# Performance work log

Hardware: AMD Instinct MI355X
Metric: run time of the kernel (lower is better)

The kernel has to match this reference:

```python
import jax, jax.numpy as jnp
import numpy as np

INPUT_DIMS = 512
OUTPUT_DIMS = 512
GRID_SIZE = 8


def setup_inputs() -> dict:
    key = jax.random.key(0)
    k_x, k_w = jax.random.split(key)
    x = jax.random.normal(k_x, (4, 2048, INPUT_DIMS), dtype=jnp.float32)
    scale = 1.0 / (np.sqrt(INPUT_DIMS) * np.sqrt(GRID_SIZE))
    fouriercoeffs = jax.random.normal(
        k_w, (2, OUTPUT_DIMS, INPUT_DIMS, GRID_SIZE), dtype=jnp.float32) * scale
    bias = jnp.zeros((1, OUTPUT_DIMS), dtype=jnp.float32)
    return {"x": x, "fouriercoeffs": fouriercoeffs, "bias": bias}


def reference(x, fouriercoeffs, bias):
    out_shape = x.shape[:-1] + (OUTPUT_DIMS,)
    xf = x.reshape(-1, INPUT_DIMS)  # [N, I]
    k = jnp.arange(1, GRID_SIZE + 1, dtype=x.dtype)  # [G]
    arg = xf[:, :, None] * k  # [N, I, G]
    # contract cos/sin features against coeffs: two batched GEMMs
    y = jnp.einsum('nig,oig->no', jnp.cos(arg), fouriercoeffs[0])
    y = y + jnp.einsum('nig,oig->no', jnp.sin(arg), fouriercoeffs[1])
    y = y + bias
    return y.reshape(out_shape)
```

## Files before the change

### kernel.cpp

```cpp
#include <hip/hip_runtime.h>
#include <hip/hip_bf16.h>


typedef __attribute__((ext_vector_type(8))) short s16x8;
typedef __attribute__((ext_vector_type(4))) int   i32x4;
typedef __attribute__((ext_vector_type(4))) float f32x4;

#define NROWS 8192
#define IDIM  512
#define ODIM  512
#define KDIM  8192

static __device__ __forceinline__ short f2bf(float f) {
    union { float f; unsigned u; } v; v.f = f;
    unsigned r = v.u + 0x7fffu + ((v.u >> 16) & 1u);
    return (short)(r >> 16);
}

static __device__ __forceinline__ float bf2f(short h) {
    union { unsigned u; float f; } v;
    v.u = ((unsigned)(unsigned short)h) << 16;
    return v.f;
}

static __device__ __forceinline__ int pkbf(float c, float s) {
    union { __hip_bfloat162 h; int i; } u;
    u.h = __float22bfloat162_rn(make_float2(c, s));
    return u.i;
}

__global__ __launch_bounds__(256) void fkan_prep(const float* __restrict__ cf,
                                                 short* __restrict__ Wb) {
    const int o = blockIdx.x;
    const int tid = threadIdx.x;
#pragma unroll
    for (int rep = 0; rep < 2; ++rep) {
        const int i = tid + rep * 256;
        const float* c0 = cf + (o * 512 + i) * 8;
        const float* c1 = cf + ((512 + o) * 512 + i) * 8;
        float4 a0 = *(const float4*)c0;
        float4 a1 = *(const float4*)(c0 + 4);
        float4 b0 = *(const float4*)c1;
        float4 b1 = *(const float4*)(c1 + 4);
        s16x8 lo, hi;
        lo[0] = f2bf(a0.x); lo[1] = f2bf(b0.x);
        lo[2] = f2bf(a0.y); lo[3] = f2bf(b0.y);
        lo[4] = f2bf(a0.z); lo[5] = f2bf(b0.z);
        lo[6] = f2bf(a0.w); lo[7] = f2bf(b0.w);
        hi[0] = f2bf(a1.x); hi[1] = f2bf(b1.x);
        hi[2] = f2bf(a1.y); hi[3] = f2bf(b1.y);
        hi[4] = f2bf(a1.z); hi[5] = f2bf(b1.z);
        hi[6] = f2bf(a1.w); hi[7] = f2bf(b1.w);
        *(s16x8*)(Wb + o * KDIM + i * 16)     = lo;
        *(s16x8*)(Wb + o * KDIM + i * 16 + 8) = hi;
    }
}

__global__ __launch_bounds__(512, 2) void fkan_gemm4(const float* __restrict__ x,
                                                     const short* __restrict__ Wb,
                                                     short* __restrict__ P) {
    __shared__ short As[2][128 * 64];
    __shared__ short Bs[2][256 * 64];

    const int bid = blockIdx.x;
    const int xcd = bid & 7;
    const int kc  = xcd >> 1;
    const int bm  = ((bid >> 3) << 1) | (xcd & 1);
    const int n0 = bm * 128;
    const int i0 = kc * 128;
    const int kbase = i0 * 16;
    const int NKT = 64;

    const int tid = threadIdx.x;
    const int wid = tid >> 6, lane = tid & 63;
    const int lrow = lane & 15, lk = lane >> 4;
    const int wr = wid >> 2, wc = wid & 3;

    f32x4 acc[4][8];
#pragma unroll
    for (int a = 0; a < 4; ++a)
#pragma unroll
        for (int b = 0; b < 8; ++b) {
            f32x4 z = {0.f, 0.f, 0.f, 0.f};
            acc[a][b] = z;
        }

    const int nl = tid >> 2, isel = tid & 3;
    const float* xrow = x + (n0 + nl) * 512 + i0 + isel;

    auto stageA = [&](short* Ab, float xx) {
        float s1, c1;
        __sincosf(xx, &s1, &c1);
        float c = c1, s = s1;
        i32x4 lo, hi;
#pragma unroll
        for (int g = 0; g < 8; ++g) {
            const int p = pkbf(c, s);
            if (g < 4) lo[g] = p; else hi[g - 4] = p;
            const float t1 = s * s1, t2 = c * s1;
            const float cn = __builtin_fmaf(c, c1, -t1);
            s = __builtin_fmaf(s, c1, t2);
            c = cn;
        }
        const int cb0 = isel * 2;
        *(i32x4*)&Ab[nl * 64 + ((cb0 ^ (nl & 7))) * 8]       = lo;
        *(i32x4*)&Ab[nl * 64 + (((cb0 + 1) ^ (nl & 7))) * 8] = hi;
    };

    auto stageB = [&](int t, int nb) {
#pragma unroll
        for (int w = 0; w < 4; ++w) {
            const int ch = w * 512 + tid;
            const int l = ch >> 3, sl = ch & 7;
            const int cb = sl ^ (l & 7);
            const int r = 2 * l + (cb >> 2);
            const short* src = Wb + (size_t)r * KDIM + kbase + t * 32 + (cb & 3) * 8;
            short* ldst = &Bs[nb][w * 4096 + wid * 512];
            __builtin_amdgcn_global_load_lds(
                (const __attribute__((address_space(1))) void*)src,
                (__attribute__((address_space(3))) void*)ldst, 16, 0, 0);
        }
    };

    float xv = xrow[0];
    stageA(As[0], xv);
    stageB(0, 0);
    xv = xrow[4];
    __syncthreads();

    for (int kt = 0; kt < NKT; ++kt) {
        const int bcur = kt & 1;
        const int abuf = (kt >> 1) & 1;

        s16x8 af[4], bfr[8];
#pragma unroll
        for (int mf = 0; mf < 4; ++mf) {
            const int row = wr * 64 + mf * 16 + lrow;
            af[mf] = *(const s16x8*)&As[abuf][row * 64 + (((kt & 1) * 4 + lk) ^ (row & 7)) * 8];
        }
#pragma unroll
        for (int nf = 0; nf < 8; ++nf) {
            const int r = wc * 128 + nf * 16 + lrow;
            const int l = r >> 1;
            const int sl = (((r & 1) * 4 + lk) ^ (l & 7));
            bfr[nf] = *(const s16x8*)&Bs[bcur][l * 64 + sl * 8];
        }

        if (kt + 1 < NKT) stageB(kt + 1, bcur ^ 1);
        if ((kt & 1) == 0 && kt + 2 < NKT) {
            stageA(As[abuf ^ 1], xv);
            if (kt + 4 < NKT) xv = xrow[((kt >> 1) + 2) * 4];
        }

        __builtin_amdgcn_s_setprio(1);
#pragma unroll
        for (int mf = 0; mf < 4; ++mf)
#pragma unroll
            for (int nf = 0; nf < 8; ++nf)
                acc[mf][nf] = __builtin_amdgcn_mfma_f32_16x16x32_bf16(
                    af[mf], bfr[nf], acc[mf][nf], 0, 0, 0);
        __builtin_amdgcn_s_setprio(0);

        __syncthreads();
    }

    unsigned short* dst = (unsigned short*)P + (size_t)kc * (NROWS * ODIM);
#pragma unroll
    for (int nf = 0; nf < 8; ++nf) {
        const int oc = wc * 128 + nf * 16 + lrow;
#pragma unroll
        for (int mf = 0; mf < 4; ++mf) {
            const f32x4 v = acc[mf][nf];
            const int rbase = n0 + wr * 64 + mf * 16 + lk * 4;
#pragma unroll
            for (int j = 0; j < 4; ++j)
                dst[(size_t)(rbase + j) * 512 + oc] = (unsigned short)f2bf(v[j]);
        }
    }
}

__global__ __launch_bounds__(256) void fkan_combine4(const short* __restrict__ P,
                                                     const float* __restrict__ bias,
                                                     float* __restrict__ out) {
    const int total = NROWS * ODIM;
    const int stride = gridDim.x * 256 * 8;
    for (int e = (blockIdx.x * 256 + threadIdx.x) * 8; e < total; e += stride) {
        s16x8 a = *(const s16x8*)(P + e);
        s16x8 b = *(const s16x8*)(P + total + e);
        s16x8 c = *(const s16x8*)(P + 2 * total + e);
        s16x8 d = *(const s16x8*)(P + 3 * total + e);
        const int col = e & 511;
        float4 c0 = *(const float4*)(bias + col);
        float4 c1 = *(const float4*)(bias + col + 4);
        float4 r0, r1;
        r0.x = (bf2f(a[0]) + bf2f(b[0])) + (bf2f(c[0]) + bf2f(d[0])) + c0.x;
        r0.y = (bf2f(a[1]) + bf2f(b[1])) + (bf2f(c[1]) + bf2f(d[1])) + c0.y;
        r0.z = (bf2f(a[2]) + bf2f(b[2])) + (bf2f(c[2]) + bf2f(d[2])) + c0.z;
        r0.w = (bf2f(a[3]) + bf2f(b[3])) + (bf2f(c[3]) + bf2f(d[3])) + c0.w;
        r1.x = (bf2f(a[4]) + bf2f(b[4])) + (bf2f(c[4]) + bf2f(d[4])) + c1.x;
        r1.y = (bf2f(a[5]) + bf2f(b[5])) + (bf2f(c[5]) + bf2f(d[5])) + c1.y;
        r1.z = (bf2f(a[6]) + bf2f(b[6])) + (bf2f(c[6]) + bf2f(d[6])) + c1.z;
        r1.w = (bf2f(a[7]) + bf2f(b[7])) + (bf2f(c[7]) + bf2f(d[7])) + c1.w;
        *(float4*)(out + e)     = r0;
        *(float4*)(out + e + 4) = r1;
    }
}

__global__ __launch_bounds__(256, 2) void fkan_gemm_fb(const float* __restrict__ x,
                                                       const short* __restrict__ Wb,
                                                       const float* __restrict__ bias,
                                                       float* __restrict__ outp) {
    __shared__ short As[2][128 * 64];
    __shared__ short Bs[2][128 * 64];
    const int bid = blockIdx.x;
    const int xcd = bid & 7, idx = bid >> 3;
    const int bn = xcd & 3, bm = idx + (xcd >> 2) * 32;
    const int n0 = bm * 128, o0 = bn * 128;
    const int tid = threadIdx.x;
    const int wid = tid >> 6, lane = tid & 63;
    const int lrow = lane & 15, lk = lane >> 4;
    const int wr = wid >> 1, wc = wid & 1;
    f32x4 acc[4][4];
#pragma unroll
    for (int a = 0; a < 4; ++a)
#pragma unroll
        for (int b = 0; b < 4; ++b) { f32x4 z = {0,0,0,0}; acc[a][b] = z; }
    const int nl = tid >> 1, isel = tid & 1;
    const float* xrow = x + (n0 + nl) * 512 + isel * 2;
    auto stage = [&](int t, int nb, float2 xvv) {
#pragma unroll
        for (int w = 0; w < 4; ++w) {
            const int chunk = w * 256 + tid;
            const int r = chunk >> 3, pc = chunk & 7;
            const int lc = pc ^ (r & 7);
            const short* src = Wb + (o0 + r) * KDIM + t * 64 + lc * 8;
            short* ldst = &Bs[nb][w * 2048 + wid * 512];
            __builtin_amdgcn_global_load_lds(
                (const __attribute__((address_space(1))) void*)src,
                (__attribute__((address_space(3))) void*)ldst, 16, 0, 0);
        }
#pragma unroll
        for (int ii = 0; ii < 2; ++ii) {
            const float xx = ii ? xvv.y : xvv.x;
            float s1, c1; __sincosf(xx, &s1, &c1);
            float c = c1, s = s1;
            i32x4 lo, hi;
#pragma unroll
            for (int g = 0; g < 8; ++g) {
                const int p = pkbf(c, s);
                if (g < 4) lo[g] = p; else hi[g - 4] = p;
                const float t1 = s * s1, t2 = c * s1;
                const float cn = __builtin_fmaf(c, c1, -t1);
                s = __builtin_fmaf(s, c1, t2); c = cn;
            }
            const int cb0 = (isel * 2 + ii) * 2;
            *(i32x4*)&As[nb][nl * 64 + ((cb0 ^ (nl & 7))) * 8]       = lo;
            *(i32x4*)&As[nb][nl * 64 + (((cb0 + 1) ^ (nl & 7))) * 8] = hi;
        }
    };
    float2 xv = *(const float2*)xrow;
    stage(0, 0, xv);
    xv = *(const float2*)(xrow + 4);
    __syncthreads();
    for (int kt = 0; kt < 128; ++kt) {
        const int cur = kt & 1;
        s16x8 af[2][4], bfr[2][4];
#pragma unroll
        for (int ksub = 0; ksub < 2; ++ksub) {
#pragma unroll
            for (int mf = 0; mf < 4; ++mf) {
                const int row = wr * 64 + mf * 16 + lrow;
                af[ksub][mf] = *(const s16x8*)&As[cur][row * 64 + ((ksub * 4 + lk) ^ (row & 7)) * 8];
            }
#pragma unroll
            for (int nf = 0; nf < 4; ++nf) {
                const int row = wc * 64 + nf * 16 + lrow;
                bfr[ksub][nf] = *(const s16x8*)&Bs[cur][row * 64 + ((ksub * 4 + lk) ^ (row & 7)) * 8];
            }
        }
        if (kt + 1 < 128) {
            stage(kt + 1, cur ^ 1, xv);
            if (kt + 2 < 128) xv = *(const float2*)(xrow + (kt + 2) * 4);
        }
#pragma unroll
        for (int ksub = 0; ksub < 2; ++ksub)
#pragma unroll
            for (int mf = 0; mf < 4; ++mf)
#pragma unroll
                for (int nf = 0; nf < 4; ++nf)
                    acc[mf][nf] = __builtin_amdgcn_mfma_f32_16x16x32_bf16(
                        af[ksub][mf], bfr[ksub][nf], acc[mf][nf], 0, 0, 0);
        __syncthreads();
    }
#pragma unroll
    for (int nf = 0; nf < 4; ++nf) {
        const int oc = o0 + wc * 64 + nf * 16 + lrow;
        const float bv = bias[oc];
#pragma unroll
        for (int mf = 0; mf < 4; ++mf) {
            const f32x4 v = acc[mf][nf];
            const int rbase = n0 + wr * 64 + mf * 16 + lk * 4;
#pragma unroll
            for (int j = 0; j < 4; ++j)
                outp[(size_t)(rbase + j) * 512 + oc] = v[j] + bv;
        }
    }
}

extern "C" void kernel_launch(void* const* d_in, const int* in_sizes, int n_in,
                              void* d_out, int out_size, void* d_ws, size_t ws_size,
                              hipStream_t stream) {
    const float* x    = (const float*)d_in[0];
    const float* cf   = (const float*)d_in[1];
    const float* bias = (const float*)d_in[2];
    float* out = (float*)d_out;

    const size_t partial_bytes = (size_t)4 * NROWS * ODIM * 2;
    const size_t wb_bytes = (size_t)ODIM * KDIM * 2;

    if (ws_size >= partial_bytes + wb_bytes) {
        short* P  = (short*)d_ws;
        short* Wb = (short*)((char*)d_ws + partial_bytes);
        fkan_prep<<<512, 256, 0, stream>>>(cf, Wb);
        fkan_gemm4<<<256, 512, 0, stream>>>(x, Wb, P);
        fkan_combine4<<<2048, 256, 0, stream>>>(P, bias, out);
    } else {
        short* Wb = (short*)d_ws;
        fkan_prep<<<512, 256, 0, stream>>>(cf, Wb);
        fkan_gemm_fb<<<256, 256, 0, stream>>>(x, Wb, bias, out);
    }
}
```

Before: 92.56 us.

## Restructure GEMM main loop with explicit waitcnt and two-stage B prefetch

Rewrites the fkan_gemm4 main loop as a manually unrolled pair of k-steps per iteration. Both B buffers are prefetched up front, and plain __syncthreads is replaced with explicit s_waitcnt vmcnt/lgkmcnt plus s_barrier and sched_barrier. The goal is for global-to-LDS loads to stay in flight longer across MFMA work instead of draining every iteration. The cost is fragile, hand-tuned vmcnt counts that must match the number of outstanding loads, so a miscount would cause races or extra stalls.

```diff
diff --git a/kernel.cpp b/kernel.cpp
--- a/kernel.cpp
+++ b/kernel.cpp
@@ -69,7 +69,6 @@
     const int n0 = bm * 128;
     const int i0 = kc * 128;
     const int kbase = i0 * 16;
-    const int NKT = 64;
 
     const int tid = threadIdx.x;
     const int wid = tid >> 6, lane = tid & 63;
@@ -122,46 +121,98 @@
         }
     };
 
-    float xv = xrow[0];
-    stageA(As[0], xv);
+    float xv0 = xrow[0];
+    float xv  = xrow[4];
+    stageA(As[0], xv0);
     stageB(0, 0);
-    xv = xrow[4];
-    __syncthreads();
-
-    for (int kt = 0; kt < NKT; ++kt) {
-        const int bcur = kt & 1;
-        const int abuf = (kt >> 1) & 1;
-
-        s16x8 af[4], bfr[8];
-#pragma unroll
-        for (int mf = 0; mf < 4; ++mf) {
-            const int row = wr * 64 + mf * 16 + lrow;
-            af[mf] = *(const s16x8*)&As[abuf][row * 64 + (((kt & 1) * 4 + lk) ^ (row & 7)) * 8];
-        }
-#pragma unroll
-        for (int nf = 0; nf < 8; ++nf) {
-            const int r = wc * 128 + nf * 16 + lrow;
-            const int l = r >> 1;
-            const int sl = (((r & 1) * 4 + lk) ^ (l & 7));
-            bfr[nf] = *(const s16x8*)&Bs[bcur][l * 64 + sl * 8];
-        }
-
-        if (kt + 1 < NKT) stageB(kt + 1, bcur ^ 1);
-        if ((kt & 1) == 0 && kt + 2 < NKT) {
-            stageA(As[abuf ^ 1], xv);
-            if (kt + 4 < NKT) xv = xrow[((kt >> 1) + 2) * 4];
-        }
-
-        __builtin_amdgcn_s_setprio(1);
-#pragma unroll
-        for (int mf = 0; mf < 4; ++mf)
-#pragma unroll
-            for (int nf = 0; nf < 8; ++nf)
-                acc[mf][nf] = __builtin_amdgcn_mfma_f32_16x16x32_bf16(
-                    af[mf], bfr[nf], acc[mf][nf], 0, 0, 0);
-        __builtin_amdgcn_s_setprio(0);
-
-        __syncthreads();
+    stageB(1, 1);
+    asm volatile("s_waitcnt vmcnt(4) lgkmcnt(0)" ::: "memory");
+    __builtin_amdgcn_sched_barrier(0);
+    __builtin_amdgcn_s_barrier();
+
+#pragma unroll 1
+    for (int kt2 = 0; kt2 < 32; ++kt2) {
+        const int kt = kt2 * 2;
+        short* Acur = As[kt2 & 1];
+        short* Anxt = As[(kt2 + 1) & 1];
+
+        {
+            s16x8 af[4], bfr[8];
+#pragma unroll
+            for (int mf = 0; mf < 4; ++mf) {
+                const int row = wr * 64 + mf * 16 + lrow;
+                af[mf] = *(const s16x8*)&Acur[row * 64 + ((lk) ^ (row & 7)) * 8];
+            }
+#pragma unroll
+            for (int nf = 0; nf < 8; ++nf) {
+                const int r = wc * 128 + nf * 16 + lrow;
+                const int l = r >> 1;
+                bfr[nf] = *(const s16x8*)&Bs[0][l * 64 + (((r & 1) * 4 + lk) ^ (l & 7)) * 8];
+            }
+            asm volatile("s_waitcnt lgkmcnt(0)" ::: "memory");
+            __builtin_amdgcn_sched_barrier(0);
+            __builtin_amdgcn_s_barrier();
+
+            if (kt2 < 31) {
+                stageB(kt + 2, 0);
+                stageA(Anxt, xv);
+                if (kt2 < 30) xv = xrow[(kt2 + 2) * 4];
+            }
+
+            __builtin_amdgcn_s_setprio(1);
+#pragma unroll
+            for (int mf = 0; mf < 4; ++mf)
+#pragma unroll
+                for (int nf = 0; nf < 8; ++nf)
+                    acc[mf][nf] = __builtin_amdgcn_mfma_f32_16x16x32_bf16(
+                        af[mf], bfr[nf], acc[mf][nf], 0, 0, 0);
+            __builtin_amdgcn_s_setprio(0);
+
+            if (kt2 < 30)
+                asm volatile("s_waitcnt vmcnt(5) lgkmcnt(0)" ::: "memory");
+            else if (kt2 == 30)
+                asm volatile("s_waitcnt vmcnt(4) lgkmcnt(0)" ::: "memory");
+            else
+                asm volatile("s_waitcnt vmcnt(0) lgkmcnt(0)" ::: "memory");
+            __builtin_amdgcn_sched_barrier(0);
+            __builtin_amdgcn_s_barrier();
+        }
+
+        {
+            s16x8 af[4], bfr[8];
+#pragma unroll
+            for (int mf = 0; mf < 4; ++mf) {
+                const int row = wr * 64 + mf * 16 + lrow;
+                af[mf] = *(const s16x8*)&Acur[row * 64 + ((4 + lk) ^ (row & 7)) * 8];
+            }
+#pragma unroll
+            for (int nf = 0; nf < 8; ++nf) {
+                const int r = wc * 128 + nf * 16 + lrow;
+                const int l = r >> 1;
+                bfr[nf] = *(const s16x8*)&Bs[1][l * 64 + (((r & 1) * 4 + lk) ^ (l & 7)) * 8];
+            }
+            asm volatile("s_waitcnt lgkmcnt(0)" ::: "memory");
+            __builtin_amdgcn_sched_barrier(0);
+            __builtin_amdgcn_s_barrier();
+
+            if (kt2 < 31) stageB(kt + 3, 1);
+
+            __builtin_amdgcn_s_setprio(1);
+#pragma unroll
+            for (int mf = 0; mf < 4; ++mf)
+#pragma unroll
+                for (int nf = 0; nf < 8; ++nf)
+                    acc[mf][nf] = __builtin_amdgcn_mfma_f32_16x16x32_bf16(
+                        af[mf], bfr[nf], acc[mf][nf], 0, 0, 0);
+            __builtin_amdgcn_s_setprio(0);
+
+            if (kt2 < 30)
+                asm volatile("s_waitcnt vmcnt(5)" ::: "memory");
+            else if (kt2 == 30)
+                asm volatile("s_waitcnt vmcnt(4)" ::: "memory");
+            __builtin_amdgcn_sched_barrier(0);
+            __builtin_amdgcn_s_barrier();
+        }
     }
 
     unsigned short* dst = (unsigned short*)P + (size_t)kc * (NROWS * ODIM);
```

Measured after the change: 91.75 us. Within noise of the previous version (-0.9%).

## Split GEMM tiles across output halves with 256-thread blocks and per-step staging

Applied to the files above, without the earlier changes.

The GEMM kernel now gives each block a 128x256 output tile instead of 128x512 and launches 512 blocks of 256 threads instead of 256 blocks of 512. The sin/cos A-tile is now produced every k-step into a padded 40-stride buffer, merged with the B load into one stage function. The set-priority hints around the MFMA loop are removed. The aim is more blocks per CU and simpler LDS indexing, at the cost of recomputing the Fourier features twice (once per output half) and loading x twice.

```diff
diff --git a/kernel.cpp b/kernel.cpp
--- a/kernel.cpp
+++ b/kernel.cpp
@@ -56,25 +56,24 @@
     }
 }
 
-__global__ __launch_bounds__(512, 2) void fkan_gemm4(const float* __restrict__ x,
+__global__ __launch_bounds__(256, 2) void fkan_gemm9(const float* __restrict__ x,
                                                      const short* __restrict__ Wb,
                                                      short* __restrict__ P) {
-    __shared__ short As[2][128 * 64];
-    __shared__ short Bs[2][256 * 64];
+    __shared__ short As[2][128 * 40];
+    __shared__ short Bs[2][256 * 32];
 
     const int bid = blockIdx.x;
     const int xcd = bid & 7;
-    const int kc  = xcd >> 1;
-    const int bm  = ((bid >> 3) << 1) | (xcd & 1);
-    const int n0 = bm * 128;
-    const int i0 = kc * 128;
+    const int bn = xcd & 1, kc = xcd >> 1;
+    const int bm = bid >> 3;
+    const int n0 = bm * 128, o0 = bn * 256, i0 = kc * 128;
     const int kbase = i0 * 16;
     const int NKT = 64;
 
     const int tid = threadIdx.x;
     const int wid = tid >> 6, lane = tid & 63;
     const int lrow = lane & 15, lk = lane >> 4;
-    const int wr = wid >> 2, wc = wid & 3;
+    const int wr = wid >> 1, wc = wid & 1;
 
     f32x4 acc[4][8];
 #pragma unroll
@@ -85,10 +84,21 @@
             acc[a][b] = z;
         }
 
-    const int nl = tid >> 2, isel = tid & 3;
+    const int nl = tid >> 1, isel = tid & 1;
     const float* xrow = x + (n0 + nl) * 512 + i0 + isel;
 
-    auto stageA = [&](short* Ab, float xx) {
+    auto stage = [&](int t, int nb, float xx) {
+#pragma unroll
+        for (int w = 0; w < 4; ++w) {
+            const int ch = w * 256 + tid;
+            const int r = ch >> 2, sl = ch & 3;
+            const int cb = sl ^ ((r >> 1) & 3);
+            const short* src = Wb + (size_t)(o0 + r) * KDIM + kbase + t * 32 + cb * 8;
+            short* ldst = &Bs[nb][w * 2048 + wid * 512];
+            __builtin_amdgcn_global_load_lds(
+                (const __attribute__((address_space(1))) void*)src,
+                (__attribute__((address_space(3))) void*)ldst, 16, 0, 0);
+        }
         float s1, c1;
         __sincosf(xx, &s1, &c1);
         float c = c1, s = s1;
@@ -102,64 +112,43 @@
             s = __builtin_fmaf(s, c1, t2);
             c = cn;
         }
-        const int cb0 = isel * 2;
-        *(i32x4*)&Ab[nl * 64 + ((cb0 ^ (nl & 7))) * 8]       = lo;
-        *(i32x4*)&Ab[nl * 64 + (((cb0 + 1) ^ (nl & 7))) * 8] = hi;
+        short* Ab = As[nb];
+        *(i32x4*)&Ab[nl * 40 + (isel * 2) * 8]     = lo;
+        *(i32x4*)&Ab[nl * 40 + (isel * 2 + 1) * 8] = hi;
     };
 
-    auto stageB = [&](int t, int nb) {
-#pragma unroll
-        for (int w = 0; w < 4; ++w) {
-            const int ch = w * 512 + tid;
-            const int l = ch >> 3, sl = ch & 7;
-            const int cb = sl ^ (l & 7);
-            const int r = 2 * l + (cb >> 2);
-            const short* src = Wb + (size_t)r * KDIM + kbase + t * 32 + (cb & 3) * 8;
-            short* ldst = &Bs[nb][w * 4096 + wid * 512];
-            __builtin_amdgcn_global_load_lds(
-                (const __attribute__((address_space(1))) void*)src,
-                (__attribute__((address_space(3))) void*)ldst, 16, 0, 0);
-        }
-    };
-
     float xv = xrow[0];
-    stageA(As[0], xv);
-    stageB(0, 0);
-    xv = xrow[4];
+    stage(0, 0, xv);
+    xv = xrow[2];
     __syncthreads();
 
     for (int kt = 0; kt < NKT; ++kt) {
-        const int bcur = kt & 1;
-        const int abuf = (kt >> 1) & 1;
+        const int cur = kt & 1;
 
         s16x8 af[4], bfr[8];
 #pragma unroll
         for (int mf = 0; mf < 4; ++mf) {
             const int row = wr * 64 + mf * 16 + lrow;
-            af[mf] = *(const s16x8*)&As[abuf][row * 64 + (((kt & 1) * 4 + lk) ^ (row & 7)) * 8];
+            af[mf] = *(const s16x8*)&As[cur][row * 40 + lk * 8];
         }
 #pragma unroll
         for (int nf = 0; nf < 8; ++nf) {
-            const int r = wc * 128 + nf * 16 + lrow;
-            const int l = r >> 1;
-            const int sl = (((r & 1) * 4 + lk) ^ (l & 7));
-            bfr[nf] = *(const s16x8*)&Bs[bcur][l * 64 + sl * 8];
-        }
-
-        if (kt + 1 < NKT) stageB(kt + 1, bcur ^ 1);
-        if ((kt & 1) == 0 && kt + 2 < NKT) {
-            stageA(As[abuf ^ 1], xv);
-            if (kt + 4 < NKT) xv = xrow[((kt >> 1) + 2) * 4];
-        }
-
-        __builtin_amdgcn_s_setprio(1);
+            const int row = wc * 128 + nf * 16 + lrow;
+            const int sl = lk ^ ((row >> 1) & 3);
+            bfr[nf] = *(const s16x8*)&Bs[cur][row * 32 + sl * 8];
+        }
+
+        if (kt + 1 < NKT) {
+            stage(kt + 1, cur ^ 1, xv);
+            if (kt + 2 < NKT) xv = xrow[(kt + 2) * 2];
+        }
+
 #pragma unroll
         for (int mf = 0; mf < 4; ++mf)
 #pragma unroll
             for (int nf = 0; nf < 8; ++nf)
                 acc[mf][nf] = __builtin_amdgcn_mfma_f32_16x16x32_bf16(
                     af[mf], bfr[nf], acc[mf][nf], 0, 0, 0);
-        __builtin_amdgcn_s_setprio(0);
 
         __syncthreads();
     }
@@ -167,7 +156,7 @@
     unsigned short* dst = (unsigned short*)P + (size_t)kc * (NROWS * ODIM);
 #pragma unroll
     for (int nf = 0; nf < 8; ++nf) {
-        const int oc = wc * 128 + nf * 16 + lrow;
+        const int oc = o0 + wc * 128 + nf * 16 + lrow;
 #pragma unroll
         for (int mf = 0; mf < 4; ++mf) {
             const f32x4 v = acc[mf][nf];
@@ -322,7 +311,7 @@
         short* P  = (short*)d_ws;
         short* Wb = (short*)((char*)d_ws + partial_bytes);
         fkan_prep<<<512, 256, 0, stream>>>(cf, Wb);
-        fkan_gemm4<<<256, 512, 0, stream>>>(x, Wb, P);
+        fkan_gemm9<<<512, 256, 0, stream>>>(x, Wb, P);
         fkan_combine4<<<2048, 256, 0, stream>>>(P, bias, out);
     } else {
         short* Wb = (short*)d_ws;
```

New measurement: 93.86 us. No clear change (+1.4%).
